# Optimization experiments

Hardware: AMD Instinct MI355X
Metric: run time of the kernel (lower is better)

The kernel has to match this reference:

```python
import jax, jax.numpy as jnp
import numpy as np

EMBED_DIM = 1024
NUM_HEADS = 16
HEAD_DIM = EMBED_DIM // NUM_HEADS


def setup_inputs() -> dict:
    key = jax.random.key(0)
    kx, kq, kk, kv, ko = jax.random.split(key, 5)
    B, S = 4, 2048
    std = 1.0 / np.sqrt(EMBED_DIM)
    x = jax.random.normal(kx, (B, S, EMBED_DIM), dtype=jnp.float32)
    # nn.Linear weights stored as [out, in]; applied as x @ W.T
    Wq = jax.random.normal(kq, (EMBED_DIM, EMBED_DIM), dtype=jnp.float32) * std
    Wk = jax.random.normal(kk, (EMBED_DIM, EMBED_DIM), dtype=jnp.float32) * std
    Wv = jax.random.normal(kv, (EMBED_DIM, EMBED_DIM), dtype=jnp.float32) * std
    Wo = jax.random.normal(ko, (EMBED_DIM, EMBED_DIM), dtype=jnp.float32) * std
    return {"x": x, "Wq": Wq, "Wk": Wk, "Wv": Wv, "Wo": Wo}


def reference(x, Wq, Wk, Wv, Wo):
    B, S, E = x.shape
    H, D = NUM_HEADS, HEAD_DIM
    scale = jnp.sqrt(jnp.float32(D))

    def proj(W):
        # x @ W.T -> (B, S, E) -> (B, H, S, D)
        return (x @ W.T).reshape(B, S, H, D).transpose(0, 2, 1, 3)

    q, k, v = proj(Wq), proj(Wk), proj(Wv)
    scores = jnp.einsum("bhsd,bhtd->bhst", q, k) / scale  # (B,H,S,S)
    causal = jnp.tril(jnp.ones((S, S), dtype=bool))
    scores = jnp.where(causal, scores, -jnp.inf)
    attn = jax.nn.softmax(scores, axis=-1)  # dropout in eval mode = identity
    out = jnp.einsum("bhst,bhtd->bhsd", attn, v)  # (B,H,S,D)
    out = out.transpose(0, 2, 1, 3).reshape(B, S, E)
    return out @ Wo.T
```

## Files before the change

kernel.cpp:

```cpp
#include <hip/hip_runtime.h>
#include <stdint.h>

#define NHEADS 16
#define EDIM   1024
#define SEQ    2048
#define BATCH  4

typedef float  floatx4 __attribute__((ext_vector_type(4)));
typedef __bf16 bf16x8  __attribute__((ext_vector_type(8)));
typedef unsigned short u16;

__device__ __forceinline__ u16 f2bf(float f) {
  union { float f; unsigned int u; } v; v.f = f;
  return (u16)((v.u + 0x7fffu + ((v.u >> 16) & 1u)) >> 16);
}

__device__ __forceinline__ unsigned int pkbf(float lo, float hi) {
  union { float f; unsigned int u; } a, c;
  a.f = lo; c.f = hi;
  return __builtin_amdgcn_perm(c.u + 0x8000u, a.u + 0x8000u, 0x07060302u);
}

__device__ __forceinline__ unsigned int cvtpk(float lo, float hi) {
  unsigned int r;
  asm("v_cvt_pk_bf16_f32 %0, %1, %2" : "=v"(r) : "v"(lo), "v"(hi));
  return r;
}

__device__ __forceinline__ void gl2lds16(const u16* g, u16* l) {
  __builtin_amdgcn_global_load_lds(
      (const __attribute__((address_space(1))) unsigned int*)g,
      (__attribute__((address_space(3))) unsigned int*)l, 16, 0, 0);
}

__global__ void cvt_all(const float* __restrict__ x,  const float* __restrict__ wq,
                        const float* __restrict__ wk, const float* __restrict__ wv,
                        const float* __restrict__ wo, u16* __restrict__ xb,
                        u16* __restrict__ wqkv, u16* __restrict__ wob, float qscale) {
  const float* src; u16* dst; int n4; float sc = 1.f;
  switch (blockIdx.y) {
    case 0: src = x;  dst = xb;             n4 = 2097152; break;
    case 1: src = wq; dst = wqkv;           n4 = 262144; sc = qscale; break;
    case 2: src = wk; dst = wqkv + 1048576; n4 = 262144; break;
    case 3: src = wv; dst = wqkv + 2097152; n4 = 262144; break;
    default: src = wo; dst = wob;           n4 = 262144; break;
  }
  const int stride = gridDim.x * blockDim.x;
  for (int i = blockIdx.x * blockDim.x + threadIdx.x; i < n4; i += stride) {
    float4 f = ((const float4*)src)[i];
    uint2 o;
    o.x = pkbf(f.x * sc, f.y * sc);
    o.y = pkbf(f.z * sc, f.w * sc);
    ((uint2*)dst)[i] = o;
  }
}

__global__ __launch_bounds__(512, 4)
void gemm_qkv(const u16* __restrict__ A, const u16* __restrict__ B,
              u16* __restrict__ Cq, u16* __restrict__ Ck, u16* __restrict__ Cv) {
  constexpr int SLOT = (128 + 256) * 32;
  constexpr int BOFF = 128 * 32;
  __shared__ __align__(16) u16 ring[3][SLOT];
  const int tid  = threadIdx.x;
  const int w    = tid >> 6, lane = tid & 63;
  const int quad = lane >> 4, l15 = lane & 15;
  const int wrow = (w >> 2) * 64, bcol = (w & 3) * 64;

  const int f  = (int)blockIdx.x;
  const int g  = f >> 3;
  const int bx = (f & 7) * 4 + (g & 3);
  const int by = g >> 2;
  const int rowA0 = by * 128, rowB0 = bx * 256;
  const int matid = rowA0 >> 10;

  const int cp = lane & 3;
  const int ra = w * 16 + (lane >> 2);
  const u16* srcA  = A + (size_t)(rowA0 + ra) * 1024 + (cp ^ ((ra >> 1) & 3)) * 8;
  const int rb0 = w * 32 + (lane >> 2);
  const u16* srcB0 = B + (size_t)(rowB0 + rb0) * 1024 + (cp ^ ((rb0 >> 1) & 3)) * 8;
  const u16* srcB1 = srcB0 + 16 * 1024;

#define STG(sl, tt)                                                          \
  {                                                                          \
    const int _ko = (tt) * 32;                                               \
    gl2lds16(srcA + _ko, &ring[sl][0] + w * 512);                            \
    gl2lds16(srcB0 + _ko, &ring[sl][BOFF] + w * 1024);                       \
    gl2lds16(srcB1 + _ko, &ring[sl][BOFF] + w * 1024 + 512);                 \
  }

  const floatx4 vzero = {0.f, 0.f, 0.f, 0.f};
  floatx4 acc[4][4];
#pragma unroll
  for (int mi = 0; mi < 4; ++mi)
#pragma unroll
    for (int ni = 0; ni < 4; ++ni) acc[mi][ni] = vzero;

  const int swz8 = (quad ^ ((l15 >> 1) & 3)) * 8;
  constexpr int NT = 32;
  STG(0, 0);
  STG(1, 1);
  int cs = 0, ss = 2;

#define KLOOP(SWAPPED)                                                       \
  for (int t = 0; t < NT; ++t) {                                             \
    if (t < NT - 1) asm volatile("s_waitcnt vmcnt(3)" ::: "memory");         \
    else            asm volatile("s_waitcnt vmcnt(0)" ::: "memory");         \
    __builtin_amdgcn_s_barrier();                                            \
    if (t + 2 < NT) { STG(ss, t + 2); ss = (ss == 2) ? 0 : ss + 1; }         \
    const u16* As = &ring[cs][0];                                            \
    const u16* Bs = &ring[cs][BOFF];                                         \
    cs = (cs == 2) ? 0 : cs + 1;                                             \
    bf16x8 af[4], bfr[4];                                                    \
    _Pragma("unroll")                                                        \
    for (int j = 0; j < 4; ++j)                                              \
      af[j] = *(const bf16x8*)(As + (wrow + j * 16 + l15) * 32 + swz8);      \
    _Pragma("unroll")                                                        \
    for (int nj = 0; nj < 4; ++nj)                                           \
      bfr[nj] = *(const bf16x8*)(Bs + (bcol + nj * 16 + l15) * 32 + swz8);   \
    __builtin_amdgcn_s_setprio(1);                                           \
    _Pragma("unroll")                                                        \
    for (int mi = 0; mi < 4; ++mi)                                           \
      _Pragma("unroll")                                                      \
      for (int ni = 0; ni < 4; ++ni) {                                       \
        if (SWAPPED)                                                         \
          acc[mi][ni] = __builtin_amdgcn_mfma_f32_16x16x32_bf16(             \
              bfr[ni], af[mi], acc[mi][ni], 0, 0, 0);                        \
        else                                                                 \
          acc[mi][ni] = __builtin_amdgcn_mfma_f32_16x16x32_bf16(             \
              af[mi], bfr[ni], acc[mi][ni], 0, 0, 0);                        \
      }                                                                      \
    __builtin_amdgcn_s_setprio(0);                                           \
  }

  if (matid < 2) {
    KLOOP(0)
    u16* dst = (matid == 0) ? Cq : Ck;
#pragma unroll
    for (int mi = 0; mi < 4; ++mi)
#pragma unroll
      for (int ni = 0; ni < 4; ++ni) {
        const int e0 = rowA0 + wrow + mi * 16 + quad * 4;
        const int s  = rowB0 + bcol + ni * 16 + l15;
        const int e_loc = e0 & 1023;
        uint2 pk;
        pk.x = pkbf(acc[mi][ni][0], acc[mi][ni][1]);
        pk.y = pkbf(acc[mi][ni][2], acc[mi][ni][3]);
        *(uint2*)(dst + (size_t)s * 1024 + e_loc) = pk;
      }
  } else {
    KLOOP(1)
#pragma unroll
    for (int mi = 0; mi < 4; ++mi)
#pragma unroll
      for (int ni = 0; ni < 4; ++ni) {
        const int e_loc = (rowA0 & 1023) + wrow + mi * 16 + l15;
        const int s_full = rowB0 + bcol + ni * 16 + quad * 4;
        const int pos = (s_full & ~31) | (quad << 3) | ((ni & 1) << 2);
        const int bb = pos >> 11, pos_loc = pos & 2047;
        uint2 pk;
        pk.x = pkbf(acc[mi][ni][0], acc[mi][ni][1]);
        pk.y = pkbf(acc[mi][ni][2], acc[mi][ni][3]);
        *(uint2*)(Cv + (size_t)(bb * 1024 + e_loc) * SEQ + pos_loc) = pk;
      }
  }
#undef KLOOP
#undef STG
}

__global__ __launch_bounds__(512, 4)
void gemm_out(const u16* __restrict__ A, const u16* __restrict__ B,
              float* __restrict__ C) {
  constexpr int SLOT = 256 * 32;
  constexpr int BOFF = 128 * 32;
  __shared__ __align__(16) u16 ring[3][SLOT];
  const int tid  = threadIdx.x;
  const int w    = tid >> 6, lane = tid & 63;
  const int quad = lane >> 4, l15 = lane & 15;
  const int wrow = (w >> 2) * 64, bcol = (w & 3) * 32;

  const int f  = (int)blockIdx.x;
  const int g  = f >> 3;
  const int bx = (f & 7) * 8 + (g & 7);
  const int by = g >> 3;
  const int rowA0 = by * 128, rowB0 = bx * 128;

  const int cp = lane & 3;
  const int ra = w * 16 + (lane >> 2);
  const u16* srcA  = A + (size_t)(rowA0 + ra) * 1024 + (cp ^ ((ra >> 1) & 3)) * 8;
  const u16* srcB0 = B + (size_t)(rowB0 + ra) * 1024 + (cp ^ ((ra >> 1) & 3)) * 8;

#define STG(sl, tt)                                                          \
  {                                                                          \
    const int _ko = (tt) * 32;                                               \
    gl2lds16(srcA + _ko, &ring[sl][0] + w * 512);                            \
    gl2lds16(srcB0 + _ko, &ring[sl][BOFF] + w * 512);                        \
  }

  const floatx4 vzero = {0.f, 0.f, 0.f, 0.f};
  floatx4 acc[4][2];
#pragma unroll
  for (int mi = 0; mi < 4; ++mi)
#pragma unroll
    for (int ni = 0; ni < 2; ++ni) acc[mi][ni] = vzero;

  const int swz8 = (quad ^ ((l15 >> 1) & 3)) * 8;
  constexpr int NT = 32;
  STG(0, 0);
  STG(1, 1);
  int cs = 0, ss = 2;

  for (int t = 0; t < NT; ++t) {
    if (t < NT - 1) asm volatile("s_waitcnt vmcnt(2)" ::: "memory");
    else            asm volatile("s_waitcnt vmcnt(0)" ::: "memory");
    __builtin_amdgcn_s_barrier();
    if (t + 2 < NT) { STG(ss, t + 2); ss = (ss == 2) ? 0 : ss + 1; }

    const u16* As = &ring[cs][0];
    const u16* Bs = &ring[cs][BOFF];
    cs = (cs == 2) ? 0 : cs + 1;
    bf16x8 af[4], bfr[2];
#pragma unroll
    for (int j = 0; j < 4; ++j)
      af[j] = *(const bf16x8*)(As + (wrow + j * 16 + l15) * 32 + swz8);
#pragma unroll
    for (int nj = 0; nj < 2; ++nj)
      bfr[nj] = *(const bf16x8*)(Bs + (bcol + nj * 16 + l15) * 32 + swz8);
    __builtin_amdgcn_s_setprio(1);
#pragma unroll
    for (int mi = 0; mi < 4; ++mi)
#pragma unroll
      for (int ni = 0; ni < 2; ++ni)
        acc[mi][ni] = __builtin_amdgcn_mfma_f32_16x16x32_bf16(af[mi], bfr[ni], acc[mi][ni], 0, 0, 0);
    __builtin_amdgcn_s_setprio(0);
  }
#undef STG

#pragma unroll
  for (int mi = 0; mi < 4; ++mi)
#pragma unroll
    for (int ni = 0; ni < 2; ++ni) {
      const int e0 = rowA0 + wrow + mi * 16 + quad * 4;
      const int s  = rowB0 + bcol + ni * 16 + l15;
      *(floatx4*)(C + (size_t)s * 1024 + e0) = acc[mi][ni];
    }
}

__global__ __launch_bounds__(512, 4)
void attn_fwd(const u16* __restrict__ Q, const u16* __restrict__ K,
              const u16* __restrict__ Vp, u16* __restrict__ Ctx) {
  __shared__ u16 SMEM[4 * 8192];
  const int tid  = threadIdx.x;
  const int w    = tid >> 6, lane = tid & 63;
  const int quad = lane >> 4, l15 = lane & 15;
  const int qg = w >> 1, tg = w & 1;
  const int bh = blockIdx.x, b = bh >> 4, h = bh & 15;
  const int qt = 15 - (int)blockIdx.y;
  const int kmax = qt;
  const int q0 = qt * 128 + qg * 32;

  bf16x8 bq[2][2];
#pragma unroll
  for (int ni = 0; ni < 2; ++ni)
#pragma unroll
    for (int ks = 0; ks < 2; ++ks) {
      const int qs = q0 + ni * 16 + l15;
      bq[ni][ks] = *(const bf16x8*)(Q + (size_t)(b * SEQ + qs) * EDIM + h * 64 + ks * 32 + quad * 8);
    }

  union { unsigned int u[4]; bf16x8 v; } ones;
  ones.u[0] = ones.u[1] = ones.u[2] = ones.u[3] = 0x3F803F80u;

  const floatx4 vzero = {0.f, 0.f, 0.f, 0.f};
  floatx4 o_acc[4][2];
  floatx4 l_vacc[2] = {vzero, vzero};
#pragma unroll
  for (int di = 0; di < 4; ++di)
#pragma unroll
    for (int ni = 0; ni < 2; ++ni) o_acc[di][ni] = vzero;

  const int krow = lane >> 3, kch = lane & 7;
  const int vrow = lane >> 4, vch = lane & 15;

#define STAGE_KV(buf, ktn)                                                          \
  {                                                                                 \
    _Pragma("unroll")                                                               \
    for (int ii = 0; ii < 2; ++ii) {                                                \
      const int r0 = w * 16 + ii * 8;                                               \
      const int row = r0 + krow;                                                    \
      gl2lds16(K + (size_t)(b * SEQ + (ktn) * 128 + row) * EDIM + h * 64 +          \
                   ((kch ^ (row & 7)) * 8),                                         \
               SMEM + (buf) * 8192 + r0 * 64);                                      \
      const int d0 = w * 8 + ii * 4;                                                \
      const int dd = d0 + vrow;                                                     \
      gl2lds16(Vp + (size_t)(bh * 64 + dd) * SEQ + (ktn) * 128 +                    \
                   ((vch ^ (dd & 15)) * 8),                                         \
               SMEM + 16384 + (buf) * 8192 + d0 * 128);                             \
    }                                                                               \
  }

  STAGE_KV(0, 0);

  for (int kt = 0; kt <= kmax; ++kt) {
    const int cur = kt & 1;
    __syncthreads();
    if (kt < kmax) STAGE_KV(cur ^ 1, kt + 1);
    const u16* Ksc = SMEM + cur * 8192;
    const u16* Vsc = SMEM + 16384 + cur * 8192;

    unsigned int pk[2][2][4];
#pragma unroll
    for (int mi = 0; mi < 4; ++mi) {
      floatx4 s[2] = {vzero, vzero};
#pragma unroll
      for (int ks = 0; ks < 2; ++ks) {
        bf16x8 ak = *(const bf16x8*)(Ksc + (tg * 64 + mi * 16 + l15) * 64 +
                                     (((ks * 4 + quad) ^ (l15 & 7)) * 8));
#pragma unroll
        for (int ni = 0; ni < 2; ++ni)
          s[ni] = __builtin_amdgcn_mfma_f32_16x16x32_bf16(ak, bq[ni][ks], s[ni], 0, 0, 0);
      }
      if (kt == kmax) {
#pragma unroll
        for (int ni = 0; ni < 2; ++ni)
#pragma unroll
          for (int r = 0; r < 4; ++r) {
            const int t_loc = tg * 64 + mi * 16 + quad * 4 + r;
            const int q_loc = qg * 32 + ni * 16 + l15;
            if (t_loc > q_loc) s[ni][r] = -1e30f;
          }
      }
#pragma unroll
      for (int ni = 0; ni < 2; ++ni) {
        float p0 = __builtin_amdgcn_exp2f(s[ni][0]);
        float p1 = __builtin_amdgcn_exp2f(s[ni][1]);
        float p2 = __builtin_amdgcn_exp2f(s[ni][2]);
        float p3 = __builtin_amdgcn_exp2f(s[ni][3]);
        pk[ni][mi >> 1][(mi & 1) * 2 + 0] = cvtpk(p0, p1);
        pk[ni][mi >> 1][(mi & 1) * 2 + 1] = cvtpk(p2, p3);
      }
    }

#pragma unroll
    for (int ks = 0; ks < 2; ++ks) {
      bf16x8 va[4];
#pragma unroll
      for (int di = 0; di < 4; ++di)
        va[di] = *(const bf16x8*)(Vsc + (di * 16 + l15) * 128 +
                                  (((tg * 8 + ks * 4 + quad) ^ l15) * 8));
#pragma unroll
      for (int ni = 0; ni < 2; ++ni) {
        union { unsigned int u[4]; bf16x8 v; } pb;
        pb.u[0] = pk[ni][ks][0]; pb.u[1] = pk[ni][ks][1];
        pb.u[2] = pk[ni][ks][2]; pb.u[3] = pk[ni][ks][3];
        l_vacc[ni] = __builtin_amdgcn_mfma_f32_16x16x32_bf16(ones.v, pb.v, l_vacc[ni], 0, 0, 0);
#pragma unroll
        for (int di = 0; di < 4; ++di)
          o_acc[di][ni] = __builtin_amdgcn_mfma_f32_16x16x32_bf16(va[di], pb.v, o_acc[di][ni], 0, 0, 0);
      }
    }
  }

  float lt[2];
#pragma unroll
  for (int ni = 0; ni < 2; ++ni) lt[ni] = l_vacc[ni][0];
  __syncthreads();
  float* red  = (float*)SMEM;
  float* lred = red + 8448;
  if (tg == 1) {
#pragma unroll
    for (int ni = 0; ni < 2; ++ni) {
#pragma unroll
      for (int di = 0; di < 4; ++di)
#pragma unroll
        for (int r = 0; r < 4; ++r)
          red[qg * 2112 + (di * 16 + quad * 4 + r) * 33 + ni * 16 + l15] = o_acc[di][ni][r];
      if (quad == 0) lred[qg * 32 + ni * 16 + l15] = lt[ni];
    }
  }
  __syncthreads();
  if (tg == 0) {
#pragma unroll
    for (int ni = 0; ni < 2; ++ni) {
      const float rl = 1.f / (lt[ni] + lred[qg * 32 + ni * 16 + l15]);
      const int qs = q0 + ni * 16 + l15;
#pragma unroll
      for (int di = 0; di < 4; ++di) {
        float v0 = (o_acc[di][ni][0] + red[qg * 2112 + (di * 16 + quad * 4 + 0) * 33 + ni * 16 + l15]) * rl;
        float v1 = (o_acc[di][ni][1] + red[qg * 2112 + (di * 16 + quad * 4 + 1) * 33 + ni * 16 + l15]) * rl;
        float v2 = (o_acc[di][ni][2] + red[qg * 2112 + (di * 16 + quad * 4 + 2) * 33 + ni * 16 + l15]) * rl;
        float v3 = (o_acc[di][ni][3] + red[qg * 2112 + (di * 16 + quad * 4 + 3) * 33 + ni * 16 + l15]) * rl;
        uint2 ov;
        ov.x = cvtpk(v0, v1);
        ov.y = cvtpk(v2, v3);
        *(uint2*)(Ctx + (size_t)(b * SEQ + qs) * EDIM + h * 64 + di * 16 + quad * 4) = ov;
      }
    }
  }
#undef STAGE_KV
}

extern "C" void kernel_launch(void* const* d_in, const int* in_sizes, int n_in,
                              void* d_out, int out_size, void* d_ws, size_t ws_size,
                              hipStream_t stream) {
  const float* x  = (const float*)d_in[0];
  const float* Wq = (const float*)d_in[1];
  const float* Wk = (const float*)d_in[2];
  const float* Wv = (const float*)d_in[3];
  const float* Wo = (const float*)d_in[4];
  float* out = (float*)d_out;
  u16* ws = (u16*)d_ws;

  const size_t ME = (size_t)BATCH * SEQ * EDIM;
  u16* Xb   = ws;
  u16* Wqkv = Xb + ME;
  u16* Wob  = Wqkv + 3u * 1024 * 1024;
  u16* Qb   = Wob + 1024u * 1024;
  u16* Kb   = Qb + ME;
  u16* Vpb  = Kb + ME;
  u16* Ctx  = Vpb + ME;

  const float qscale = 0.125f * 1.44269504f;

  cvt_all<<<dim3(512, 5), 256, 0, stream>>>(x, Wq, Wk, Wv, Wo, Xb, Wqkv, Wob, qscale);
  gemm_qkv<<<dim3(768), 512, 0, stream>>>(Wqkv, Xb, Qb, Kb, Vpb);
  attn_fwd<<<dim3(64, 16), 512, 0, stream>>>(Qb, Kb, Vpb, Ctx);
  gemm_out<<<dim3(512), 512, 0, stream>>>(Wob, Ctx, out);
}
```

Before: 216.7 us.

## Give each attention wave its own query rows and double the query tile

The attention kernel now assigns each of the 8 waves a distinct 32-row query slice of a 256-row query tile, instead of pairing waves that split the key tile and then merge partial results through shared memory. Each wave processes all 128 keys per tile and skips key tiles lying entirely above its causal diagonal, so the cross-wave reduction and its barriers go away. Each staged K/V tile is reused by twice as many query rows, but the grid is halved and waves within a block get unequal amounts of work near the diagonal. That imbalance and the doubled per-wave P register footprint may hurt occupancy or load balance.

After: 238.0 us. 1.1x slower.

```diff
diff --git a/kernel.cpp b/kernel.cpp
--- a/kernel.cpp
+++ b/kernel.cpp
@@ -252,11 +252,11 @@
   const int tid  = threadIdx.x;
   const int w    = tid >> 6, lane = tid & 63;
   const int quad = lane >> 4, l15 = lane & 15;
-  const int qg = w >> 1, tg = w & 1;
+  const int qg = w;
   const int bh = blockIdx.x, b = bh >> 4, h = bh & 15;
-  const int qt = 15 - (int)blockIdx.y;
-  const int kmax = qt;
-  const int q0 = qt * 128 + qg * 32;
+  const int qt = 7 - (int)blockIdx.y;
+  const int kmax = 2 * qt + 1;
+  const int q0 = qt * 256 + qg * 32;
 
   bf16x8 bq[2][2];
 #pragma unroll
@@ -307,93 +307,74 @@
     const u16* Ksc = SMEM + cur * 8192;
     const u16* Vsc = SMEM + 16384 + cur * 8192;
 
-    unsigned int pk[2][2][4];
-#pragma unroll
-    for (int mi = 0; mi < 4; ++mi) {
-      floatx4 s[2] = {vzero, vzero};
-#pragma unroll
-      for (int ks = 0; ks < 2; ++ks) {
-        bf16x8 ak = *(const bf16x8*)(Ksc + (tg * 64 + mi * 16 + l15) * 64 +
-                                     (((ks * 4 + quad) ^ (l15 & 7)) * 8));
-#pragma unroll
-        for (int ni = 0; ni < 2; ++ni)
-          s[ni] = __builtin_amdgcn_mfma_f32_16x16x32_bf16(ak, bq[ni][ks], s[ni], 0, 0, 0);
+    const int tbase = kt * 128 - qt * 256;
+    if (tbase <= qg * 32 + 31) {
+      const bool needmask = (tbase + 127) > (qg * 32);
+
+      unsigned int pk[2][4][4];
+#pragma unroll
+      for (int mi = 0; mi < 8; ++mi) {
+        floatx4 s[2] = {vzero, vzero};
+#pragma unroll
+        for (int ks = 0; ks < 2; ++ks) {
+          bf16x8 ak = *(const bf16x8*)(Ksc + (mi * 16 + l15) * 64 +
+                                       (((ks * 4 + quad) ^ (l15 & 7)) * 8));
+#pragma unroll
+          for (int ni = 0; ni < 2; ++ni)
+            s[ni] = __builtin_amdgcn_mfma_f32_16x16x32_bf16(ak, bq[ni][ks], s[ni], 0, 0, 0);
+        }
+        if (needmask) {
+#pragma unroll
+          for (int ni = 0; ni < 2; ++ni)
+#pragma unroll
+            for (int r = 0; r < 4; ++r) {
+              const int t_loc = tbase + mi * 16 + quad * 4 + r;
+              const int q_loc = qg * 32 + ni * 16 + l15;
+              if (t_loc > q_loc) s[ni][r] = -1e30f;
+            }
+        }
+#pragma unroll
+        for (int ni = 0; ni < 2; ++ni) {
+          float p0 = __builtin_amdgcn_exp2f(s[ni][0]);
+          float p1 = __builtin_amdgcn_exp2f(s[ni][1]);
+          float p2 = __builtin_amdgcn_exp2f(s[ni][2]);
+          float p3 = __builtin_amdgcn_exp2f(s[ni][3]);
+          pk[ni][mi >> 1][(mi & 1) * 2 + 0] = cvtpk(p0, p1);
+          pk[ni][mi >> 1][(mi & 1) * 2 + 1] = cvtpk(p2, p3);
+        }
       }
-      if (kt == kmax) {
-#pragma unroll
-        for (int ni = 0; ni < 2; ++ni)
-#pragma unroll
-          for (int r = 0; r < 4; ++r) {
-            const int t_loc = tg * 64 + mi * 16 + quad * 4 + r;
-            const int q_loc = qg * 32 + ni * 16 + l15;
-            if (t_loc > q_loc) s[ni][r] = -1e30f;
-          }
-      }
-#pragma unroll
-      for (int ni = 0; ni < 2; ++ni) {
-        float p0 = __builtin_amdgcn_exp2f(s[ni][0]);
-        float p1 = __builtin_amdgcn_exp2f(s[ni][1]);
-        float p2 = __builtin_amdgcn_exp2f(s[ni][2]);
-        float p3 = __builtin_amdgcn_exp2f(s[ni][3]);
-        pk[ni][mi >> 1][(mi & 1) * 2 + 0] = cvtpk(p0, p1);
-        pk[ni][mi >> 1][(mi & 1) * 2 + 1] = cvtpk(p2, p3);
+
+#pragma unroll
+      for (int ks = 0; ks < 4; ++ks) {
+        bf16x8 va[4];
+#pragma unroll
+        for (int di = 0; di < 4; ++di)
+          va[di] = *(const bf16x8*)(Vsc + (di * 16 + l15) * 128 +
+                                    (((ks * 4 + quad) ^ l15) * 8));
+#pragma unroll
+        for (int ni = 0; ni < 2; ++ni) {
+          union { unsigned int u[4]; bf16x8 v; } pb;
+          pb.u[0] = pk[ni][ks][0]; pb.u[1] = pk[ni][ks][1];
+          pb.u[2] = pk[ni][ks][2]; pb.u[3] = pk[ni][ks][3];
+          l_vacc[ni] = __builtin_amdgcn_mfma_f32_16x16x32_bf16(ones.v, pb.v, l_vacc[ni], 0, 0, 0);
+#pragma unroll
+          for (int di = 0; di < 4; ++di)
+            o_acc[di][ni] = __builtin_amdgcn_mfma_f32_16x16x32_bf16(va[di], pb.v, o_acc[di][ni], 0, 0, 0);
+        }
       }
     }
-
-#pragma unroll
-    for (int ks = 0; ks < 2; ++ks) {
-      bf16x8 va[4];
-#pragma unroll
-      for (int di = 0; di < 4; ++di)
-        va[di] = *(const bf16x8*)(Vsc + (di * 16 + l15) * 128 +
-                                  (((tg * 8 + ks * 4 + quad) ^ l15) * 8));
-#pragma unroll
-      for (int ni = 0; ni < 2; ++ni) {
-        union { unsigned int u[4]; bf16x8 v; } pb;
-        pb.u[0] = pk[ni][ks][0]; pb.u[1] = pk[ni][ks][1];
-        pb.u[2] = pk[ni][ks][2]; pb.u[3] = pk[ni][ks][3];
-        l_vacc[ni] = __builtin_amdgcn_mfma_f32_16x16x32_bf16(ones.v, pb.v, l_vacc[ni], 0, 0, 0);
-#pragma unroll
-        for (int di = 0; di < 4; ++di)
-          o_acc[di][ni] = __builtin_amdgcn_mfma_f32_16x16x32_bf16(va[di], pb.v, o_acc[di][ni], 0, 0, 0);
-      }
-    }
-  }
-
-  float lt[2];
-#pragma unroll
-  for (int ni = 0; ni < 2; ++ni) lt[ni] = l_vacc[ni][0];
-  __syncthreads();
-  float* red  = (float*)SMEM;
-  float* lred = red + 8448;
-  if (tg == 1) {
-#pragma unroll
-    for (int ni = 0; ni < 2; ++ni) {
-#pragma unroll
-      for (int di = 0; di < 4; ++di)
-#pragma unroll
-        for (int r = 0; r < 4; ++r)
-          red[qg * 2112 + (di * 16 + quad * 4 + r) * 33 + ni * 16 + l15] = o_acc[di][ni][r];
-      if (quad == 0) lred[qg * 32 + ni * 16 + l15] = lt[ni];
-    }
-  }
-  __syncthreads();
-  if (tg == 0) {
-#pragma unroll
-    for (int ni = 0; ni < 2; ++ni) {
-      const float rl = 1.f / (lt[ni] + lred[qg * 32 + ni * 16 + l15]);
-      const int qs = q0 + ni * 16 + l15;
-#pragma unroll
-      for (int di = 0; di < 4; ++di) {
-        float v0 = (o_acc[di][ni][0] + red[qg * 2112 + (di * 16 + quad * 4 + 0) * 33 + ni * 16 + l15]) * rl;
-        float v1 = (o_acc[di][ni][1] + red[qg * 2112 + (di * 16 + quad * 4 + 1) * 33 + ni * 16 + l15]) * rl;
-        float v2 = (o_acc[di][ni][2] + red[qg * 2112 + (di * 16 + quad * 4 + 2) * 33 + ni * 16 + l15]) * rl;
-        float v3 = (o_acc[di][ni][3] + red[qg * 2112 + (di * 16 + quad * 4 + 3) * 33 + ni * 16 + l15]) * rl;
-        uint2 ov;
-        ov.x = cvtpk(v0, v1);
-        ov.y = cvtpk(v2, v3);
-        *(uint2*)(Ctx + (size_t)(b * SEQ + qs) * EDIM + h * 64 + di * 16 + quad * 4) = ov;
-      }
+  }
+
+#pragma unroll
+  for (int ni = 0; ni < 2; ++ni) {
+    const float rl = 1.f / l_vacc[ni][0];
+    const int qs = q0 + ni * 16 + l15;
+#pragma unroll
+    for (int di = 0; di < 4; ++di) {
+      uint2 ov;
+      ov.x = cvtpk(o_acc[di][ni][0] * rl, o_acc[di][ni][1] * rl);
+      ov.y = cvtpk(o_acc[di][ni][2] * rl, o_acc[di][ni][3] * rl);
+      *(uint2*)(Ctx + (size_t)(b * SEQ + qs) * EDIM + h * 64 + di * 16 + quad * 4) = ov;
     }
   }
 #undef STAGE_KV
@@ -423,6 +404,6 @@
 
   cvt_all<<<dim3(512, 5), 256, 0, stream>>>(x, Wq, Wk, Wv, Wo, Xb, Wqkv, Wob, qscale);
   gemm_qkv<<<dim3(768), 512, 0, stream>>>(Wqkv, Xb, Qb, Kb, Vpb);
-  attn_fwd<<<dim3(64, 16), 512, 0, stream>>>(Qb, Kb, Vpb, Ctx);
+  attn_fwd<<<dim3(64, 8), 512, 0, stream>>>(Qb, Kb, Vpb, Ctx);
   gemm_out<<<dim3(512), 512, 0, stream>>>(Wob, Ctx, out);
 }
```
